# Kernel tuning notes

Measured on AMD Instinct MI355X. Metric: run time of the kernel, lower is better.

The kernel has to match this reference:

```python
import jax, jax.numpy as jnp
import numpy as np
from jax import lax


def setup_inputs() -> dict:
    key = jax.random.key(0)
    ks = jax.random.split(key, 9)
    B = 4096
    x = jax.random.normal(ks[0], (B, 1, 28, 28), jnp.float32)

    def init(k, shape, fan_in):
        return (jax.random.normal(k, shape, jnp.float32) / np.float32(np.sqrt(fan_in)))

    W1 = init(ks[1], (32, 1, 3, 3), 1 * 9)
    b1 = init(ks[2], (32,), 1 * 9)
    W2 = init(ks[3], (64, 32, 3, 3), 32 * 9)
    b2 = init(ks[4], (64,), 32 * 9)
    Wl1 = init(ks[5], (14 * 14 * 64, 128), 14 * 14 * 64)
    bl1 = init(ks[6], (128,), 14 * 14 * 64)
    Wl2 = init(ks[7], (128, 10), 128)
    bl2 = init(ks[8], (10,), 128)
    return {"x": x, "W1": W1, "b1": b1, "W2": W2, "b2": b2,
            "Wl1": Wl1, "bl1": bl1, "Wl2": Wl2, "bl2": bl2}


def _conv_same(h, W, b):
    # submanifold sparse conv == SAME-padded dense conv, output restricted to active sites
    y = lax.conv_general_dilated(h, W, window_strides=(1, 1), padding="SAME",
                                 dimension_numbers=("NCHW", "OIHW", "NCHW"))
    return y + b[None, :, None, None]


def reference(x, W1, b1, W2, b2, Wl1, bl1, Wl2, bl2):
    # active-site mask from Voxels.from_dense (nonzero pixels); submanifold convs keep it fixed
    mask = (jnp.abs(x) > 0).any(axis=1, keepdims=True).astype(x.dtype)  # [B,1,28,28]
    h = jax.nn.relu(_conv_same(x, W1, b1) * mask)   # [B,32,28,28]
    h = jax.nn.relu(_conv_same(h, W2, b2) * mask)   # [B,64,28,28]
    # sparse 2x2/2 max pool; inactive sites are 0 and post-ReLU actives are >=0,
    # so dense window max == sparse max, and all-inactive windows densify to 0
    B = h.shape[0]
    h = h.reshape(B, 64, 14, 2, 14, 2).max(axis=(3, 5))  # [B,64,14,14]
    h = h.reshape(B, 64 * 14 * 14)
    # dropout is identity in eval
    h = jax.nn.relu(h @ Wl1 + bl1)
    logits = h @ Wl2 + bl2
    return jax.nn.log_softmax(logits, axis=1)
```

## Files before the change

kernel.cpp:

```cpp
#include <hip/hip_runtime.h>
#include <math.h>

typedef __bf16 bf16;
typedef __bf16 bf16x4 __attribute__((ext_vector_type(4)));
typedef __bf16 bf16x8 __attribute__((ext_vector_type(8)));
typedef unsigned short u16;
typedef unsigned short u16x4 __attribute__((ext_vector_type(4)));
typedef unsigned short u16x8 __attribute__((ext_vector_type(8)));
typedef float f32x4 __attribute__((ext_vector_type(4)));
typedef float f32x16 __attribute__((ext_vector_type(16)));
typedef unsigned int u32x4 __attribute__((ext_vector_type(4)));

__global__ void prep_all(const float* __restrict__ W2, bf16* __restrict__ w2r,
                         const float* __restrict__ W1, bf16* __restrict__ w1f,
                         const float* __restrict__ Wl1, bf16* __restrict__ wl1t) {
    __shared__ float tile[32 * 129];
    const int b = blockIdx.x;
    const int t = threadIdx.x;
    if (b < 392) {
        const int s  = b >> 1;
        const int cg = b & 1;
        for (int e = t; e < 4096; e += 256) {
            int cl = e >> 7, n = e & 127;
            tile[cl * 129 + n] = Wl1[((long)(cg * 32 + cl) * 196 + s) * 128 + n];
        }
        __syncthreads();
        for (int e = t; e < 4096; e += 256) {
            int n = e >> 5, cl = e & 31;
            wl1t[(long)n * 12544 + s * 64 + cg * 32 + cl] = (bf16)tile[cl * 129 + n];
        }
    } else {
        int e = (b - 392) * 256 + t;
        if (e < 18432) {
            int j  = e & 7;
            int l  = (e >> 3) & 63;
            int f  = e >> 9;
            int s  = f >> 1;
            int nt = f & 1;
            int tap  = s >> 1;
            int ci   = (s & 1) * 16 + (l >> 5) * 8 + j;
            int cout = nt * 32 + (l & 31);
            w2r[e] = (bf16)W2[cout * 288 + ci * 9 + tap];
        } else {
            int e2 = e - 18432;
            if (e2 < 512) {
                int j = e2 & 7;
                int l = e2 >> 3;
                int k = (l >> 5) * 8 + j;
                int n = l & 31;
                w1f[e2] = (k < 9) ? (bf16)W1[n * 9 + k] : (bf16)0.f;
            }
        }
    }
}

__global__ __launch_bounds__(256, 3)
void conv_fused(const float* __restrict__ x, const float* __restrict__ b1,
                const bf16* __restrict__ w2r, const bf16* __restrict__ w1f,
                const float* __restrict__ b2, bf16* __restrict__ pooled)
{
    __shared__ __attribute__((aligned(16))) bf16  h1s[16 * 1024];
    __shared__ __attribute__((aligned(16))) float mneg[98 * 4];
    __shared__ __attribute__((aligned(16))) bf16  xs[640];

    const int t    = threadIdx.x;
    const int lane = t & 63;
    const int wv   = t >> 6;
    const int img  = blockIdx.x >> 1;
    const int hb   = blockIdx.x & 1;
    const int nt   = wv & 1;
    const int wp   = wv >> 1;
    const int ml31 = lane & 31;
    const int lg   = lane >> 5;

    const float* xi = x + img * 784;

    bf16x8 breg[18];
    {
        const bf16x8* wp2 = (const bf16x8*)w2r;
        #pragma unroll
        for (int s = 0; s < 18; s++)
            breg[s] = wp2[(2 * s + nt) * 64 + lane];
    }
    const bf16x8 w1frag = *(const bf16x8*)&w1f[lane * 8];
    const float  bias2  = b2[nt * 32 + ml31];
    f32x4 bq[4];
    #pragma unroll
    for (int run = 0; run < 4; run++)
        bq[run] = *(const f32x4*)&b1[4 * lg + 8 * run];

    for (int e = t; e < 640; e += 256) {
        int j  = e >> 5;
        int c  = e & 31;
        int xr = hb * 14 - 2 + j;
        int xc = c - 1;
        float v = 0.f;
        if (xr >= 0 && xr < 28 && xc >= 0 && xc < 28) v = xi[xr * 28 + xc];
        xs[e] = (bf16)v;
    }
    __syncthreads();

    const u16* xu = (const u16*)xs;

    for (int e = t; e < 392; e += 256) {
        int s   = e >> 2, q = e & 3;
        int spi = s / 14, spj = s - spi * 14;
        u16 cv = xu[(2 * spi + (q >> 1) + 2) * 32 + 2 * spj + (q & 1) + 1];
        mneg[e] = ((cv & 0x7fff) != 0) ? 0.f : -1e30f;
    }

    #pragma unroll 1
    for (int Mt = wv; Mt < 16; Mt += 4) {
        const int bb = Mt * 32 + ml31 - 1;
        u16x8 tv;
        if (lg == 0) {
            tv[0] = xu[bb];      tv[1] = xu[bb + 1];  tv[2] = xu[bb + 2];
            tv[3] = xu[bb + 32]; tv[4] = xu[bb + 33]; tv[5] = xu[bb + 34];
            tv[6] = xu[bb + 64]; tv[7] = xu[bb + 65];
        } else {
            #pragma unroll
            for (int j = 0; j < 8; j++) tv[j] = 0;
            tv[0] = xu[bb + 66];
        }
        bf16x8 af = *(bf16x8*)&tv;

        f32x16 acc;
        #pragma unroll
        for (int run = 0; run < 4; run++)
            #pragma unroll
            for (int j = 0; j < 4; j++) acc[run * 4 + j] = bq[run][j];
        acc = __builtin_amdgcn_mfma_f32_32x32x16_bf16(w1frag, af, acc, 0, 0, 0);

        u16 ctr = xu[(Mt + 1) * 32 + ml31];
        const bool ok = (ml31 >= 1) && (ml31 <= 28) && ((ctr & 0x7fff) != 0);
        const int hi2w  = ((ml31 >> 1) ^ Mt) & 3;
        const int wbase = (Mt << 10) + ml31 * 32 + 4 * lg;
        #pragma unroll
        for (int run = 0; run < 4; run++) {
            bf16x4 w4;
            #pragma unroll
            for (int j = 0; j < 4; j++) {
                float s = acc[run * 4 + j];
                w4[j] = (bf16)(ok ? fmaxf(s, 0.f) : 0.f);
            }
            *(bf16x4*)&h1s[wbase + 8 * (run ^ hi2w)] = w4;
        }
    }
    __syncthreads();

    const int cib = lg * 8;

    int q  = ml31 & 3;
    int pj = wp * 8 + (ml31 >> 2);
    int pi = 0;
    if (pj >= 14) { pj -= 14; pi = 1; }

    bf16* pout = pooled + (long)img * 12544 + hb * 98 * 64 + nt * 32 + ml31;

    #pragma unroll 1
    for (int Mt = wp; Mt < 13; Mt += 2) {
        int row = 2 * pi + (q >> 1);
        if (row > 13) row = 13;
        int colb = 2 * pj + (q & 1);

        f32x16 accE, accO;
        #pragma unroll
        for (int e = 0; e < 16; e++) { accE[e] = bias2; accO[e] = 0.f; }

        #pragma unroll
        for (int dr = 0; dr < 3; dr++) {
            const int R  = row + dr;
            const int rb = R << 10;
            #pragma unroll
            for (int dc = 0; dc < 3; dc++) {
                const int tap  = dr * 3 + dc;
                const int cc   = colb + dc;
                const int sw   = (((cc >> 1) ^ R) & 3) << 3;
                const int base = rb + cc * 32;
                bf16x8 a0 = *(const bf16x8*)&h1s[base + (cib ^ sw)];
                bf16x8 a1 = *(const bf16x8*)&h1s[base + ((16 + cib) ^ sw)];
                accE = __builtin_amdgcn_mfma_f32_32x32x16_bf16(a0, breg[2 * tap],     accE, 0, 0, 0);
                accO = __builtin_amdgcn_mfma_f32_32x32x16_bf16(a1, breg[2 * tap + 1], accO, 0, 0, 0);
            }
        }

        int slg = 8 * Mt + lg;
        #pragma unroll
        for (int gg = 0; gg < 4; gg++) {
            if (slg < 98) {
                f32x4 mn = *(const f32x4*)&mneg[slg * 4];
                float v0 = accE[gg * 4 + 0] + accO[gg * 4 + 0] + mn[0];
                float v1 = accE[gg * 4 + 1] + accO[gg * 4 + 1] + mn[1];
                float v2 = accE[gg * 4 + 2] + accO[gg * 4 + 2] + mn[2];
                float v3 = accE[gg * 4 + 3] + accO[gg * 4 + 3] + mn[3];
                float pm = fmaxf(fmaxf(v0, v1), fmaxf(v2, v3));
                pout[slg * 64] = (bf16)fmaxf(pm, 0.f);
            }
            slg += 2;
        }

        pj += 2; if (pj >= 14) { pj -= 14; pi += 1; }
        pi += 1;
    }
}

__global__ __launch_bounds__(256, 4)
void fc1(const bf16* __restrict__ pooled, const bf16* __restrict__ wl1t,
         float* __restrict__ part)
{
    __shared__ __attribute__((aligned(16))) bf16 As[2][32 * 64];
    __shared__ __attribute__((aligned(16))) bf16 Bs[2][128 * 64];

    const int t    = threadIdx.x;
    const int lane = t & 63;
    const int wv   = t >> 6;
    const int ml   = lane & 15;
    const int kg   = lane >> 4;
    const int wm   = wv & 1;
    const int wn   = wv >> 1;
    const int m0   = blockIdx.x * 32;
    const int ks   = blockIdx.y;
    const int k0   = ks * 1792;

    const bf16* asrc;
    {
        int sub = t >> 7, i = t & 127;
        int r  = i >> 2;
        int jq = (i & 3) ^ ((r >> 1) & 3);
        asrc = pooled + (long)(m0 + r) * 12544 + k0 + sub * 32 + jq * 8;
    }
    const bf16* bsrc[4];
    #pragma unroll
    for (int u = 0; u < 4; u++) {
        int c  = u * 256 + t;
        int sub = c >> 9, i = c & 511;
        int r  = i >> 2;
        int jq = (i & 3) ^ ((r >> 1) & 3);
        bsrc[u] = wl1t + (long)r * 12544 + k0 + sub * 32 + jq * 8;
    }

    const int am = wm * 16 + ml;
    int aoff[2], boff[4];
    #pragma unroll
    for (int s = 0; s < 2; s++)
        aoff[s] = s * 1024 + ((am * 32 + kg * 8) ^ ((am & 6) << 2));
    #pragma unroll
    for (int j = 0; j < 4; j++) {
        int n = wn * 64 + j * 16 + ml;
        boff[j] = (n * 32 + kg * 8) ^ ((n & 6) << 2);
    }

    f32x4 acc[4];
    {
        f32x4 z = {0.f, 0.f, 0.f, 0.f};
        #pragma unroll
        for (int j = 0; j < 4; j++) acc[j] = z;
    }

    u32x4 ra = *(const u32x4*)asrc;
    u32x4 rb[4];
    #pragma unroll
    for (int u = 0; u < 4; u++) rb[u] = *(const u32x4*)bsrc[u];
    *(u32x4*)&As[0][t * 8] = ra;
    #pragma unroll
    for (int u = 0; u < 4; u++) *(u32x4*)&Bs[0][(u * 256 + t) * 8] = rb[u];

    for (int kt = 0; kt < 28; kt++) {
        __syncthreads();
        const int cur = kt & 1;
        if (kt < 27) {
            const int kb = (kt + 1) * 64;
            ra = *(const u32x4*)(asrc + kb);
            #pragma unroll
            for (int u = 0; u < 4; u++) rb[u] = *(const u32x4*)(bsrc[u] + kb);
        }
        #pragma unroll
        for (int s = 0; s < 2; s++) {
            bf16x8 af = *(const bf16x8*)&As[cur][aoff[s]];
            #pragma unroll
            for (int j = 0; j < 4; j++) {
                bf16x8 bf = *(const bf16x8*)&Bs[cur][s * 4096 + boff[j]];
                acc[j] = __builtin_amdgcn_mfma_f32_16x16x32_bf16(af, bf, acc[j], 0, 0, 0);
            }
        }
        if (kt < 27) {
            *(u32x4*)&As[cur ^ 1][t * 8] = ra;
            #pragma unroll
            for (int u = 0; u < 4; u++)
                *(u32x4*)&Bs[cur ^ 1][(u * 256 + t) * 8] = rb[u];
        }
    }

    float* pp = part + ((long)ks * 4096 + m0 + wm * 16) * 128 + wn * 64;
    #pragma unroll
    for (int j = 0; j < 4; j++)
        #pragma unroll
        for (int r = 0; r < 4; r++)
            pp[(kg * 4 + r) * 128 + j * 16 + ml] = acc[j][r];
}

__global__ __launch_bounds__(256)
void fc2_lsm(const float* __restrict__ part, const float* __restrict__ bl1,
             const float* __restrict__ Wl2, const float* __restrict__ bl2,
             float* __restrict__ out)
{
    const int wv   = threadIdx.x >> 6;
    const int lane = threadIdx.x & 63;
    const int img  = blockIdx.x * 4 + wv;
    const float* pb = part + (long)img * 128;

    float ac[10];
    #pragma unroll
    for (int c = 0; c < 10; c++) ac[c] = 0.f;

    #pragma unroll
    for (int u = 0; u < 2; u++) {
        int n = lane + 64 * u;
        float s = bl1[n];
        #pragma unroll
        for (int k = 0; k < 7; k++) s += pb[(long)k * 4096 * 128 + n];
        float h = s > 0.f ? s : 0.f;
        #pragma unroll
        for (int c = 0; c < 10; c++) ac[c] += h * Wl2[n * 10 + c];
    }
    #pragma unroll
    for (int o = 32; o > 0; o >>= 1)
        #pragma unroll
        for (int c = 0; c < 10; c++) ac[c] += __shfl_down(ac[c], o, 64);

    if (lane == 0) {
        float lg[10], mx = -1e30f;
        #pragma unroll
        for (int c = 0; c < 10; c++) {
            lg[c] = ac[c] + bl2[c];
            mx = lg[c] > mx ? lg[c] : mx;
        }
        float se = 0.f;
        #pragma unroll
        for (int c = 0; c < 10; c++) se += __expf(lg[c] - mx);
        float ls = __logf(se);
        #pragma unroll
        for (int c = 0; c < 10; c++) out[img * 10 + c] = lg[c] - mx - ls;
    }
}

extern "C" void kernel_launch(void* const* d_in, const int* in_sizes, int n_in,
                              void* d_out, int out_size, void* d_ws, size_t ws_size,
                              hipStream_t stream) {
    const float* x   = (const float*)d_in[0];
    const float* W1  = (const float*)d_in[1];
    const float* b1  = (const float*)d_in[2];
    const float* W2  = (const float*)d_in[3];
    const float* b2  = (const float*)d_in[4];
    const float* Wl1 = (const float*)d_in[5];
    const float* bl1 = (const float*)d_in[6];
    const float* Wl2 = (const float*)d_in[7];
    const float* bl2 = (const float*)d_in[8];
    float* out = (float*)d_out;

    char* ws = (char*)d_ws;
    bf16*  w2r    = (bf16*)ws;
    bf16*  w1f    = (bf16*)(ws + 40960);
    bf16*  wl1t   = (bf16*)(ws + 65536);
    bf16*  pooled = (bf16*)(ws + 65536 + 4194304);
    float* part   = (float*)(ws + 65536 + 4194304 + 102760448);

    prep_all  <<<466,            256, 0, stream>>>(W2, w2r, W1, w1f, Wl1, wl1t);
    conv_fused<<<8192,           256, 0, stream>>>(x, b1, w2r, w1f, b2, pooled);
    fc1       <<<dim3(128, 7),   256, 0, stream>>>(pooled, wl1t, part);
    fc2_lsm   <<<1024,           256, 0, stream>>>(part, bl1, Wl2, bl2, out);
}
```

Before: 265.5 us.

## Drop LDS staging in fc1 and load MFMA operands directly from global memory

The fc1 GEMM kernel no longer stages A and B tiles through double-buffered shared memory with block barriers. Each wave now loads its bf16x8 MFMA fragments straight from global memory, and the loop is unrolled by two. This removes LDS traffic and __syncthreads, but each B tile is now fetched by both M-waves and each A tile by both N-waves, so reuse depends on the cache. The direct loads also read 16-byte pieces from rows strided by 12544 elements, which may coalesce poorly.

```diff
diff --git a/kernel.cpp b/kernel.cpp
--- a/kernel.cpp
+++ b/kernel.cpp
@@ -208,9 +208,6 @@
 void fc1(const bf16* __restrict__ pooled, const bf16* __restrict__ wl1t,
          float* __restrict__ part)
 {
-    __shared__ __attribute__((aligned(16))) bf16 As[2][32 * 64];
-    __shared__ __attribute__((aligned(16))) bf16 Bs[2][128 * 64];
-
     const int t    = threadIdx.x;
     const int lane = t & 63;
     const int wv   = t >> 6;
@@ -222,33 +219,12 @@
     const int ks   = blockIdx.y;
     const int k0   = ks * 1792;
 
-    const bf16* asrc;
-    {
-        int sub = t >> 7, i = t & 127;
-        int r  = i >> 2;
-        int jq = (i & 3) ^ ((r >> 1) & 3);
-        asrc = pooled + (long)(m0 + r) * 12544 + k0 + sub * 32 + jq * 8;
-    }
-    const bf16* bsrc[4];
-    #pragma unroll
-    for (int u = 0; u < 4; u++) {
-        int c  = u * 256 + t;
-        int sub = c >> 9, i = c & 511;
-        int r  = i >> 2;
-        int jq = (i & 3) ^ ((r >> 1) & 3);
-        bsrc[u] = wl1t + (long)r * 12544 + k0 + sub * 32 + jq * 8;
-    }
-
     const int am = wm * 16 + ml;
-    int aoff[2], boff[4];
-    #pragma unroll
-    for (int s = 0; s < 2; s++)
-        aoff[s] = s * 1024 + ((am * 32 + kg * 8) ^ ((am & 6) << 2));
-    #pragma unroll
-    for (int j = 0; j < 4; j++) {
-        int n = wn * 64 + j * 16 + ml;
-        boff[j] = (n * 32 + kg * 8) ^ ((n & 6) << 2);
-    }
+    const bf16* ap = pooled + (long)(m0 + am) * 12544 + k0 + kg * 8;
+    const bf16* bp0 = wl1t + (long)(wn * 64 + 0 * 16 + ml) * 12544 + k0 + kg * 8;
+    const bf16* bp1 = wl1t + (long)(wn * 64 + 1 * 16 + ml) * 12544 + k0 + kg * 8;
+    const bf16* bp2 = wl1t + (long)(wn * 64 + 2 * 16 + ml) * 12544 + k0 + kg * 8;
+    const bf16* bp3 = wl1t + (long)(wn * 64 + 3 * 16 + ml) * 12544 + k0 + kg * 8;
 
     f32x4 acc[4];
     {
@@ -257,37 +233,17 @@
         for (int j = 0; j < 4; j++) acc[j] = z;
     }
 
-    u32x4 ra = *(const u32x4*)asrc;
-    u32x4 rb[4];
-    #pragma unroll
-    for (int u = 0; u < 4; u++) rb[u] = *(const u32x4*)bsrc[u];
-    *(u32x4*)&As[0][t * 8] = ra;
-    #pragma unroll
-    for (int u = 0; u < 4; u++) *(u32x4*)&Bs[0][(u * 256 + t) * 8] = rb[u];
-
+    #pragma unroll 2
     for (int kt = 0; kt < 28; kt++) {
-        __syncthreads();
-        const int cur = kt & 1;
-        if (kt < 27) {
-            const int kb = (kt + 1) * 64;
-            ra = *(const u32x4*)(asrc + kb);
-            #pragma unroll
-            for (int u = 0; u < 4; u++) rb[u] = *(const u32x4*)(bsrc[u] + kb);
-        }
+        const int kb = kt * 64;
         #pragma unroll
         for (int s = 0; s < 2; s++) {
-            bf16x8 af = *(const bf16x8*)&As[cur][aoff[s]];
-            #pragma unroll
-            for (int j = 0; j < 4; j++) {
-                bf16x8 bf = *(const bf16x8*)&Bs[cur][s * 4096 + boff[j]];
-                acc[j] = __builtin_amdgcn_mfma_f32_16x16x32_bf16(af, bf, acc[j], 0, 0, 0);
-            }
-        }
-        if (kt < 27) {
-            *(u32x4*)&As[cur ^ 1][t * 8] = ra;
-            #pragma unroll
-            for (int u = 0; u < 4; u++)
-                *(u32x4*)&Bs[cur ^ 1][(u * 256 + t) * 8] = rb[u];
+            const int ko = kb + s * 32;
+            bf16x8 af = *(const bf16x8*)(ap + ko);
+            acc[0] = __builtin_amdgcn_mfma_f32_16x16x32_bf16(af, *(const bf16x8*)(bp0 + ko), acc[0], 0, 0, 0);
+            acc[1] = __builtin_amdgcn_mfma_f32_16x16x32_bf16(af, *(const bf16x8*)(bp1 + ko), acc[1], 0, 0, 0);
+            acc[2] = __builtin_amdgcn_mfma_f32_16x16x32_bf16(af, *(const bf16x8*)(bp2 + ko), acc[2], 0, 0, 0);
+            acc[3] = __builtin_amdgcn_mfma_f32_16x16x32_bf16(af, *(const bf16x8*)(bp3 + ko), acc[3], 0, 0, 0);
         }
     }
 
```

After: 353.0 us. 1.33x slower.
